# Performance work log

Measured on AMD Instinct MI355X. Metric: run time of the kernel, lower is better.

The kernel has to match this reference:

```python
import jax, jax.numpy as jnp
import numpy as np


def _gru(x, h, Wih, Whh, bih, bhh):
    # torch.nn.GRUCell math. x:(1,in), h:(1,H), Wih:(3H,in), Whh:(3H,H)
    gi = x @ Wih.T + bih
    gh = h @ Whh.T + bhh
    i_r, i_z, i_n = jnp.split(gi, 3, axis=-1)
    h_r, h_z, h_n = jnp.split(gh, 3, axis=-1)
    r = jax.nn.sigmoid(i_r + h_r)
    z = jax.nn.sigmoid(i_z + h_z)
    n = jnp.tanh(i_n + r * h_n)
    return (1.0 - z) * n + z * h


def _combine(S, Wa, ba, va):
    # SelfAttention.combine: additive attention over the stack axis.
    # S:(k,1,H), Wa:(H,A), ba:(A,), va:(A,)
    e = jnp.tanh(S @ Wa + ba) @ va          # (k,1) energies
    w = jax.nn.softmax(e, axis=0)            # softmax over stacked hidden states
    return jnp.sum(w[..., None] * S, axis=0)  # (1,H)


def setup_inputs() -> dict:
    key = jax.random.key(0)
    ks = jax.random.split(key, 20)
    T, F, H, A, L = 16384, 2048, 16, 64, 6
    G = 3 * H
    s = 0.1  # weight scale for numerical sanity
    return {
        "batch": jax.random.normal(ks[0], (T, 1, F), jnp.float32),
        "h0": jax.random.normal(ks[1], (L, 1, H), jnp.float32),
        "W_ih0": jax.random.normal(ks[2], (G, F), jnp.float32) * s,
        "W_hh0": jax.random.normal(ks[3], (G, H), jnp.float32) * s,
        "b_ih0": jax.random.normal(ks[4], (G,), jnp.float32) * s,
        "b_hh0": jax.random.normal(ks[5], (G,), jnp.float32) * s,
        "W_ih": jax.random.normal(ks[6], (L - 1, G, H), jnp.float32) * s,
        "W_hh": jax.random.normal(ks[7], (L - 1, G, H), jnp.float32) * s,
        "b_ih": jax.random.normal(ks[8], (L - 1, G), jnp.float32) * s,
        "b_hh": jax.random.normal(ks[9], (L - 1, G), jnp.float32) * s,
        "Wa": jax.random.normal(ks[10], (L, H, A), jnp.float32) * s,
        "ba": jax.random.normal(ks[11], (L, A), jnp.float32) * s,
        "va": jax.random.normal(ks[12], (L, A), jnp.float32) * s,
        "fc1_w": jax.random.normal(ks[13], (32, H), jnp.float32) * s,
        "fc1_b": jax.random.normal(ks[14], (32,), jnp.float32) * s,
        "fc2_w": jax.random.normal(ks[15], (1, 32), jnp.float32) * s,
        "fc2_b": jax.random.normal(ks[16], (1,), jnp.float32) * s,
    }


def reference(batch, h0, W_ih0, W_hh0, b_ih0, b_hh0, W_ih, W_hh, b_ih, b_hh,
              Wa, ba, va, fc1_w, fc1_b, fc2_w, fc2_b):
    L = Wa.shape[0]

    def step(h_s, x):
        # h_s: (L,1,H) carried hidden states, x: (1,F) current token
        inp = x.reshape(1, -1)
        new = []
        for l in range(L):
            if l == 0:
                inp = _gru(inp, h_s[0], W_ih0, W_hh0, b_ih0, b_hh0)
            else:
                inp = _gru(inp, h_s[l], W_ih[l - 1], W_hh[l - 1], b_ih[l - 1], b_hh[l - 1])
            new.append(inp)
        newS = jnp.stack(new)  # (L,1,H)
        # layer i attends over hidden states of layers i..L-1 (feedback combine)
        h_next = jnp.stack([_combine(newS[i:], Wa[i], ba[i], va[i]) for i in range(L)])
        top = h_next[-1].reshape(-1)  # (H,); dropout is identity in eval mode
        out = (top @ fc1_w.T + fc1_b) @ fc2_w.T + fc2_b  # (1,)
        return h_next, out

    _, outs = jax.lax.scan(step, h0, batch)
    return outs  # (T,1)
```

## Files before the change

kernel.cpp:

```cpp
#include <hip/hip_runtime.h>
#include <cstdint>
#include <cstddef>


#define TT 16384
#define FF 2048
#define HH 16
#define LL 6
#define GG 48
#define CHUNK 64
#define LOG2E 1.44269504088896340736f

__device__ float g_gi0p[(TT + CHUNK) * 64];

__device__ __forceinline__ float exp2_(float x) { return __builtin_amdgcn_exp2f(x); }
__device__ __forceinline__ float rcp_(float x) { return __builtin_amdgcn_rcpf(x); }
__device__ __forceinline__ float sig_n(float s) { return rcp_(1.f + exp2_(s)); }
__device__ __forceinline__ float tanh_p(float s) { return fmaf(-2.f, rcp_(exp2_(s) + 1.f), 1.f); }

#define MEMBAR() __asm__ __volatile__("" ::: "memory")

__device__ __forceinline__ float rdlane(float v, int l) {
  union { float f; int i; } a, b;
  a.f = v; b.i = __builtin_amdgcn_readlane(a.i, l); return b.f;
}
template <int CTRL>
__device__ __forceinline__ float dppf(float v) {
  union { float f; int i; } a, b;
  a.f = v; b.i = __builtin_amdgcn_mov_dpp(a.i, CTRL, 0xF, 0xF, true); return b.f;
}
template <int Q>
__device__ __forceinline__ float qbcast(float v) { return dppf<Q | (Q << 2) | (Q << 4) | (Q << 6)>(v); }

__device__ __forceinline__ float rowsum16(float v) {
  v += dppf<0xB1>(v);
  v += dppf<0x4E>(v);
  v += dppf<0x141>(v);
  v += dppf<0x140>(v);
  return v;
}
__device__ __forceinline__ float dot16r(const float (&w)[16], const float (&h)[16]) {
  float s0 = w[0] * h[0], s1 = w[1] * h[1], s2 = w[2] * h[2], s3 = w[3] * h[3];
#pragma unroll
  for (int k = 4; k < 16; k += 4) {
    s0 = fmaf(w[k], h[k], s0);       s1 = fmaf(w[k + 1], h[k + 1], s1);
    s2 = fmaf(w[k + 2], h[k + 2], s2); s3 = fmaf(w[k + 3], h[k + 3], s3);
  }
  return (s0 + s1) + (s2 + s3);
}
__device__ __forceinline__ float dot16i(const float (&w)[16], const float (&h)[16], float init) {
  float s0 = fmaf(w[0], h[0], init), s1 = w[1] * h[1], s2 = w[2] * h[2], s3 = w[3] * h[3];
#pragma unroll
  for (int k = 4; k < 16; k += 4) {
    s0 = fmaf(w[k], h[k], s0);       s1 = fmaf(w[k + 1], h[k + 1], s1);
    s2 = fmaf(w[k + 2], h[k + 2], s2); s3 = fmaf(w[k + 3], h[k + 3], s3);
  }
  return (s0 + s1) + (s2 + s3);
}

__device__ __forceinline__ int ldAcq(int* f) {
  return __hip_atomic_load(f, __ATOMIC_ACQUIRE, __HIP_MEMORY_SCOPE_WORKGROUP);
}
__device__ __forceinline__ void pollGE(int* f, int target) {
  while (ldAcq(f) < target) {}
}
__device__ __forceinline__ void waitFlag(int* f, int& cache, int need) {
  if (cache < need) { do { cache = ldAcq(f); } while (cache < need); }
}
__device__ __forceinline__ void sigRel(int* f, int v) {
  __hip_atomic_store(f, v, __ATOMIC_RELAXED, __HIP_MEMORY_SCOPE_WORKGROUP);
}

__device__ __forceinline__ void combBlock(const float4 A0, const float4 A1, const float4 A2,
                                          const float4 A3, float nsv,
                                          const float (&Wa)[16], float ba, float va,
                                          const float (&Wh)[16],
                                          float& S, float& ha, float& Pa) {
  float nr[16] = {A0.x, A0.y, A0.z, A0.w, A1.x, A1.y, A1.z, A1.w,
                  A2.x, A2.y, A2.z, A2.w, A3.x, A3.y, A3.z, A3.w};
  float u = dot16i(Wa, nr, ba);
  float P = dot16r(Wh, nr);
  float pe = va * tanh_p(u);
  float r = rowsum16(pe);
  float e = (rdlane(r, 0) + rdlane(r, 16)) + (rdlane(r, 32) + rdlane(r, 48));
  float w = exp2_(e);
  S += w; ha = fmaf(w, nsv, ha); Pa = fmaf(w, P, Pa);
}

__global__ __launch_bounds__(256) void gi0_gemm(const float* __restrict__ X,
                                                const float* __restrict__ W,
                                                const float* __restrict__ bias) {
  __shared__ float xs[64][132];
  __shared__ float ws[48][132];
  const int tid = threadIdx.x;
  const int t0 = blockIdx.x * 64;
  const int tg = tid & 15;
  const int tt = tid >> 4;
  float acc[4][3];
#pragma unroll
  for (int u = 0; u < 4; ++u)
#pragma unroll
    for (int v = 0; v < 3; ++v) acc[u][v] = 0.f;

  for (int k0 = 0; k0 < FF; k0 += 128) {
#pragma unroll
    for (int i = 0; i < 32; ++i) {
      int e = tid + 256 * i; int r = e >> 7, c = e & 127;
      xs[r][c] = X[(size_t)(t0 + r) * FF + k0 + c];
    }
#pragma unroll
    for (int i = 0; i < 24; ++i) {
      int e = tid + 256 * i; int r = e >> 7, c = e & 127;
      ws[r][c] = W[(size_t)r * FF + k0 + c];
    }
    __syncthreads();
#pragma unroll 8
    for (int c = 0; c < 128; ++c) {
      float x0 = xs[tt][c], x1 = xs[tt + 16][c], x2 = xs[tt + 32][c], x3 = xs[tt + 48][c];
      float w0 = ws[tg][c], w1 = ws[tg + 16][c], w2 = ws[tg + 32][c];
      acc[0][0] += x0 * w0; acc[0][1] += x0 * w1; acc[0][2] += x0 * w2;
      acc[1][0] += x1 * w0; acc[1][1] += x1 * w1; acc[1][2] += x1 * w2;
      acc[2][0] += x2 * w0; acc[2][1] += x2 * w1; acc[2][2] += x2 * w2;
      acc[3][0] += x3 * w0; acc[3][1] += x3 * w1; acc[3][2] += x3 * w2;
    }
    __syncthreads();
  }
  const float gsc3[3] = {-LOG2E, -LOG2E, 2.f * LOG2E};
#pragma unroll
  for (int u = 0; u < 4; ++u)
#pragma unroll
    for (int v = 0; v < 3; ++v)
      g_gi0p[(size_t)(t0 + tt + 16 * u) * 64 + tg * 4 + v] =
          (acc[u][v] + bias[tg + 16 * v]) * gsc3[v];
}

__global__ __launch_bounds__(512, 1) void fbrnn_scan(
    const float* __restrict__ h0,
    const float* __restrict__ Whh0, const float* __restrict__ bhh0,
    const float* __restrict__ Wih, const float* __restrict__ Whh,
    const float* __restrict__ bih, const float* __restrict__ bhh,
    const float* __restrict__ Wa, const float* __restrict__ ba,
    const float* __restrict__ va,
    const float* __restrict__ fc1w, const float* __restrict__ fc1b,
    const float* __restrict__ fc2w, const float* __restrict__ fc2b,
    float* __restrict__ out) {
  __shared__ __align__(16) float nsS[2][LL * HH];
  __shared__ __align__(16) float4 recS[5 * 64];
  __shared__ __align__(16) float4 partS[3 * 64];
  __shared__ __align__(16) float nsOut[256 * HH];
  __shared__ __align__(16) float chunkS[2][CHUNK * 64];
  __shared__ int flagNs;
  __shared__ int flagChunk;
  __shared__ int flagOut;
  __shared__ int gen5[2];

  const int tid = threadIdx.x;
  const int wv = tid >> 6;
  const int lane = tid & 63;
  const int qg = lane & 3;
  const int kk = lane >> 2;
  const int gate = (qg < 3 ? qg : 2);
  const int G = gate * 16 + kk;
  const float gsc = (gate == 2) ? 2.f * LOG2E : -LOG2E;

  const bool isChain = (wv == 0);
  const bool isStream = (wv == 4);
  const bool isFc = (wv == 6);
  const bool isComb = !isChain && !isStream && !isFc;
  const int pRow = (wv == 1) ? 0 : (wv == 2) ? 1 : (wv == 3) ? 2 : (wv == 7) ? 3 : 4;
  const int hRow = (wv == 5) ? 1 : (wv == 7) ? 2 : (wv == 6) ? 0 : -1;

  float WBih[5][16], bihR[5];
  float WB5[16];  float bhh5R = 0.f;
  float WaP[16], WhP[16];
  float baP = 0.f, vaP = 0.f, bhhP = 0.f;
  float WaH[16], WhH[16];
  float baH = 0.f, vaH = 0.f;
  float fc1R[16];
  float fb1 = 0.f, fw2 = 0.f, fb2 = 0.f;

  if (isChain) {
#pragma unroll
    for (int l = 0; l < 5; ++l) {
#pragma unroll
      for (int k = 0; k < 16; ++k) WBih[l][k] = Wih[((l * GG) + G) * 16 + k] * gsc;
      bihR[l] = bih[l * GG + G] * gsc;
    }
#pragma unroll
    for (int k = 0; k < 16; ++k) WB5[k] = Whh[(4 * GG + G) * 16 + k] * gsc;
    bhh5R = bhh[4 * GG + G] * gsc;
  }
  if (isComb) {
#pragma unroll
    for (int k = 0; k < 16; ++k) WaP[k] = Wa[(pRow * 16 + k) * 64 + lane] * (2.f * LOG2E);
    baP = ba[pRow * 64 + lane] * (2.f * LOG2E);
    vaP = va[pRow * 64 + lane] * LOG2E;
    const float* ws = (pRow == 0) ? (Whh0 + G * 16) : (Whh + ((pRow - 1) * GG + G) * 16);
#pragma unroll
    for (int k = 0; k < 16; ++k) WhP[k] = ws[k] * gsc;
    bhhP = ((pRow == 0) ? bhh0[G] : bhh[(pRow - 1) * GG + G]) * gsc;
  }
  if (hRow >= 0) {
#pragma unroll
    for (int k = 0; k < 16; ++k) WaH[k] = Wa[(hRow * 16 + k) * 64 + lane] * (2.f * LOG2E);
    baH = ba[hRow * 64 + lane] * (2.f * LOG2E);
    vaH = va[hRow * 64 + lane] * LOG2E;
    const float* ws = (hRow == 0) ? (Whh0 + G * 16) : (Whh + ((hRow - 1) * GG + G) * 16);
#pragma unroll
    for (int k = 0; k < 16; ++k) WhH[k] = ws[k] * gsc;
  }
  if (isFc) {
    const int m = lane & 31;
#pragma unroll
    for (int k = 0; k < 16; ++k) fc1R[k] = fc1w[m * 16 + k];
    fb1 = fc1b[m]; fw2 = fc2w[m]; fb2 = fc2b[0];
  }

  if (tid == 0) { flagNs = 0; flagChunk = 1; flagOut = 0; gen5[0] = 0; gen5[1] = 0; }

  float hv5 = 0.f, gh5reg = 0.f;
  if (isChain) {
    hv5 = h0[5 * 16 + kk];
    float hr[16];
#pragma unroll
    for (int k = 0; k < 16; ++k) hr[k] = h0[5 * 16 + k];
    gh5reg = dot16i(WB5, hr, bhh5R);
  } else if (isComb) {
    float hr[16];
#pragma unroll
    for (int k = 0; k < 16; ++k) hr[k] = h0[pRow * 16 + k];
    float4 rr;
    rr.x = dot16i(WhP, hr, bhhP);
    rr.y = h0[pRow * 16 + kk];
    rr.z = __int_as_float(0);
    rr.w = 0.f;
    recS[pRow * 64 + lane] = rr;
  } else if (isStream) {
    const float4* src = (const float4*)g_gi0p;
    float4* dst = (float4*)(&chunkS[0][0]);
#pragma unroll
    for (int q = 0; q < 16; ++q) dst[q * 64 + lane] = src[q * 64 + lane];
  }
  if (wv == 6) partS[0 * 64 + lane] = make_float4(0.f, 0.f, 0.f, __int_as_float(0));
  if (wv == 5) partS[1 * 64 + lane] = make_float4(0.f, 0.f, 0.f, __int_as_float(0));
  if (wv == 7) partS[2 * 64 + lane] = make_float4(0.f, 0.f, 0.f, __int_as_float(0));
  __syncthreads();

#define EBLOCK(J, WaX, baX, vaX, WhX, Sx, hax, Pax) do {                          \
    waitFlag(&flagNs, fcache, t * 8 + (J) + 1);                                   \
    const float4* np_ = (const float4*)&nsS[nb][(J) * 16];                        \
    float4 A0_ = np_[0], A1_ = np_[1], A2_ = np_[2], A3_ = np_[3];                \
    float nsv_ = nsS[nb][(J) * 16 + kk];                                          \
    combBlock(A0_, A1_, A2_, A3_, nsv_, WaX, baX, vaX, WhX, Sx, hax, Pax);        \
  } while (0)

  if (isStream) {
#pragma unroll 1
    for (int c = 1; c < 256; ++c) {
      if (c >= 2) pollGE(&flagNs, ((c - 1) * 64 - 1) * 8 + 1);
      const float4* src = (const float4*)(g_gi0p + ((size_t)c << 12));
      float4* dst = (float4*)(&chunkS[c & 1][0]);
#pragma unroll
      for (int q = 0; q < 16; ++q) dst[q * 64 + lane] = src[q * 64 + lane];
      MEMBAR();
      sigRel(&flagChunk, c + 1);
    }
    return;
  }

  if (isFc) {
    int fcache = 0;
#pragma unroll 1
    for (int t = 0; t < TT; ++t) {
      const int nb = t & 1;
      float Sh = 0.f, hah = 0.f, Pah = 0.f;
      EBLOCK(0, WaH, baH, vaH, WhH, Sh, hah, Pah);
      EBLOCK(1, WaH, baH, vaH, WhH, Sh, hah, Pah);
      EBLOCK(2, WaH, baH, vaH, WhH, Sh, hah, Pah);
      partS[0 * 64 + lane] = make_float4(Sh, hah, Pah, __int_as_float(t + 1));
      waitFlag(&flagNs, fcache, t * 8 + 6);
      const float4* np = (const float4*)(nsOut + (t & 255) * 16);
      float4 a0 = np[0], a1 = np[1], a2 = np[2], a3 = np[3];
      float nr[16] = {a0.x, a0.y, a0.z, a0.w, a1.x, a1.y, a1.z, a1.w,
                      a2.x, a2.y, a2.z, a2.w, a3.x, a3.y, a3.z, a3.w};
      float y = dot16i(fc1R, nr, fb1);
      float p = rowsum16(y * fw2);
      float o = rdlane(p, 0) + rdlane(p, 16) + fb2;
      if (lane == 0) out[t] = o;
      MEMBAR();
      sigRel(&flagOut, t + 1);
    }
    return;
  }

  if (isComb) {
    int fcache = 0;
    if (wv == 5) {
#pragma unroll 1
      for (int t = 0; t < TT; ++t) {
        const int nb = t & 1;
        const int tgt = t + 1;
        float Sh = 0.f, hah = 0.f, Pah = 0.f;
        EBLOCK(1, WaH, baH, vaH, WhH, Sh, hah, Pah);
        EBLOCK(2, WaH, baH, vaH, WhH, Sh, hah, Pah);
        partS[1 * 64 + lane] = make_float4(Sh, hah, Pah, __int_as_float(tgt));
        float S = 0.f, ha = 0.f, Pa = 0.f;
        EBLOCK(4, WaP, baP, vaP, WhP, S, ha, Pa);
        float4 A0, A1, A2, A3; float nsv5;
        for (;;) {
          int g5 = ldAcq(&gen5[nb]);
          MEMBAR();
          const float4* np = (const float4*)&nsS[nb][5 * 16];
          A0 = np[0]; A1 = np[1]; A2 = np[2]; A3 = np[3];
          nsv5 = nsS[nb][5 * 16 + kk];
          MEMBAR();
          if (g5 >= tgt) break;
        }
        combBlock(A0, A1, A2, A3, nsv5, WaP, baP, vaP, WhP, S, ha, Pa);
        const float inv = rcp_(S);
        float4 rr; rr.x = fmaf(Pa, inv, bhhP); rr.y = ha * inv;
        rr.z = __int_as_float(tgt); rr.w = 0.f;
        recS[4 * 64 + lane] = rr;
      }
    } else if (wv == 7) {
#pragma unroll 1
      for (int t = 0; t < TT; ++t) {
        const int nb = t & 1;
        const int tgt = t + 1;
        float Sh = 0.f, hah = 0.f, Pah = 0.f;
        EBLOCK(2, WaH, baH, vaH, WhH, Sh, hah, Pah);
        partS[2 * 64 + lane] = make_float4(Sh, hah, Pah, __int_as_float(tgt));
        float S = 0.f, ha = 0.f, Pa = 0.f;
        EBLOCK(3, WaP, baP, vaP, WhP, S, ha, Pa);
        EBLOCK(4, WaP, baP, vaP, WhP, S, ha, Pa);
        float4 A0, A1, A2, A3; float nsv5;
        for (;;) {
          int g5 = ldAcq(&gen5[nb]);
          MEMBAR();
          const float4* np = (const float4*)&nsS[nb][5 * 16];
          A0 = np[0]; A1 = np[1]; A2 = np[2]; A3 = np[3];
          nsv5 = nsS[nb][5 * 16 + kk];
          MEMBAR();
          if (g5 >= tgt) break;
        }
        combBlock(A0, A1, A2, A3, nsv5, WaP, baP, vaP, WhP, S, ha, Pa);
        const float inv = rcp_(S);
        float4 rr; rr.x = fmaf(Pa, inv, bhhP); rr.y = ha * inv;
        rr.z = __int_as_float(tgt); rr.w = 0.f;
        recS[3 * 64 + lane] = rr;
      }
    } else {
#pragma unroll 1
      for (int t = 0; t < TT; ++t) {
        const int nb = t & 1;
        const int tgt = t + 1;
        float S = 0.f, ha = 0.f, Pa = 0.f;
        EBLOCK(3, WaP, baP, vaP, WhP, S, ha, Pa);
        EBLOCK(4, WaP, baP, vaP, WhP, S, ha, Pa);
        float4 A0, A1, A2, A3, pp; float nsv5;
        for (;;) {
          int g5 = ldAcq(&gen5[nb]);
          MEMBAR();
          const float4* np = (const float4*)&nsS[nb][5 * 16];
          A0 = np[0]; A1 = np[1]; A2 = np[2]; A3 = np[3];
          nsv5 = nsS[nb][5 * 16 + kk];
          pp = partS[pRow * 64 + lane];
          MEMBAR();
          int pok = __all(__float_as_int(pp.w) >= tgt);
          if ((g5 >= tgt) & pok) break;
        }
        combBlock(A0, A1, A2, A3, nsv5, WaP, baP, vaP, WhP, S, ha, Pa);
        S += pp.x; ha += pp.y; Pa += pp.z;
        const float inv = rcp_(S);
        float4 rr; rr.x = fmaf(Pa, inv, bhhP); rr.y = ha * inv;
        rr.z = __int_as_float(tgt); rr.w = 0.f;
        recS[pRow * 64 + lane] = rr;
      }
    }
    return;
  }

  float gnext = chunkS[0][lane];
  float ns_sg[16];
#pragma unroll 1
  for (int t = 0; t < TT; ++t) {
    const int wb = t & 1;

    float4 r0, r1, r2, r3, r4;
    for (;;) {
      MEMBAR();
      r0 = recS[0 * 64 + lane]; r1 = recS[1 * 64 + lane]; r2 = recS[2 * 64 + lane];
      r3 = recS[3 * 64 + lane]; r4 = recS[4 * 64 + lane];
      MEMBAR();
      int c = (__float_as_int(r0.z) >= t) & (__float_as_int(r1.z) >= t) &
              (__float_as_int(r2.z) >= t) & (__float_as_int(r3.z) >= t) &
              (__float_as_int(r4.z) >= t);
      if (__all(c)) break;
    }
    float ghv[6], hv[6];
    ghv[0] = r0.x; hv[0] = r0.y; ghv[1] = r1.x; hv[1] = r1.y;
    ghv[2] = r2.x; hv[2] = r2.y; ghv[3] = r3.x; hv[3] = r3.y;
    ghv[4] = r4.x; hv[4] = r4.y;
    ghv[5] = gh5reg; hv[5] = hv5;

    if ((t & 63) == 63) {
      const int cn = (t + 1) >> 6;
      if (cn < 256) pollGE(&flagChunk, cn + 1);
    }
    if ((t & 63) == 32) pollGE(&flagOut, t - 64);
    const float gpre = chunkS[((t + 1) >> 6) & 1][((t + 1) & 63) * 64 + lane];

    float ghb[6];
#pragma unroll
    for (int l = 1; l < 6; ++l) ghb[l] = ghv[l] + bihR[l - 1];

    float gi0v = gnext;
    float ns = 0.f;
#pragma unroll
    for (int l = 0; l < 6; ++l) {
      const float gh_g = ghv[l];
      const float s = (l == 0) ? (gi0v + gh_g) : dot16i(WBih[l - 1], ns_sg, ghb[l]);
      const float sg = sig_n(s);
      const float smg = s - gh_g;
      const float sr = qbcast<0>(sg);
      const float sz = qbcast<1>(sg);
      const float a = sz * hv[l];
      const float b = 1.f - sz;
      const float tq = tanh_p(fmaf(sr, gh_g, smg));
      ns = fmaf(tq, b, a);
      if (qg == 2) {
        nsS[wb][l * 16 + kk] = ns;
        if (l == 5) nsOut[(t & 255) * 16 + kk] = ns;
      }
      MEMBAR();
      if (l == 5 && lane == 0) { sigRel(&gen5[wb], t + 1); sigRel(&flagNs, t * 8 + 6); }
#pragma unroll
      for (int k = 0; k < 16; ++k) ns_sg[k] = rdlane(ns, 4 * k + 2);
      if (l < 5 && lane == 0) sigRel(&flagNs, t * 8 + l + 1);
    }
    hv5 = qbcast<2>(ns);
    gh5reg = dot16i(WB5, ns_sg, bhh5R);
    gnext = gpre;
  }
}

extern "C" void kernel_launch(void* const* d_in, const int* in_sizes, int n_in,
                              void* d_out, int out_size, void* d_ws, size_t ws_size,
                              hipStream_t stream) {
  const float* batch = (const float*)d_in[0];
  const float* h0    = (const float*)d_in[1];
  const float* Wih0  = (const float*)d_in[2];
  const float* Whh0  = (const float*)d_in[3];
  const float* bih0  = (const float*)d_in[4];
  const float* bhh0  = (const float*)d_in[5];
  const float* Wih   = (const float*)d_in[6];
  const float* Whh   = (const float*)d_in[7];
  const float* bih   = (const float*)d_in[8];
  const float* bhh   = (const float*)d_in[9];
  const float* Wa    = (const float*)d_in[10];
  const float* ba    = (const float*)d_in[11];
  const float* va    = (const float*)d_in[12];
  const float* fc1w  = (const float*)d_in[13];
  const float* fc1b  = (const float*)d_in[14];
  const float* fc2w  = (const float*)d_in[15];
  const float* fc2b  = (const float*)d_in[16];
  float* out = (float*)d_out;
  (void)in_sizes; (void)n_in; (void)out_size; (void)d_ws; (void)ws_size;

  gi0_gemm<<<TT / 64, 256, 0, stream>>>(batch, Wih0, bih0);
  fbrnn_scan<<<1, 512, 0, stream>>>(h0, Whh0, bhh0, Wih, Whh, bih, bhh,
                                    Wa, ba, va, fc1w, fc1b, fc2w, fc2b, out);
}
```

Baseline: 24.99 ms.

## Finalize combine rows 0-1 in chain wave and rebalance partial-sum waves

Moves the final attention-combine step for rows 0 and 1 into the chain wave itself, using the layer-5 state it just computed plus partial sums posted by helper waves. This removes the handoff through shared memory for the rows needed first in the next timestep. The remaining row readiness checks are deferred until layer 2, and the chunk and output polls are moved after layer 0, so waiting overlaps with compute. The bih biases are also folded into the recurrent biases ahead of time. In exchange the chain wave does more per-step work and holds more registers, and the wave-to-row assignments are reshuffled.

```diff
diff --git a/kernel.cpp b/kernel.cpp
--- a/kernel.cpp
+++ b/kernel.cpp
@@ -146,7 +146,7 @@
     float* __restrict__ out) {
   __shared__ __align__(16) float nsS[2][LL * HH];
   __shared__ __align__(16) float4 recS[5 * 64];
-  __shared__ __align__(16) float4 partS[3 * 64];
+  __shared__ __align__(16) float4 partS[4 * 64];
   __shared__ __align__(16) float nsOut[256 * HH];
   __shared__ __align__(16) float chunkS[2][CHUNK * 64];
   __shared__ int flagNs;
@@ -166,12 +166,15 @@
   const bool isChain = (wv == 0);
   const bool isStream = (wv == 4);
   const bool isFc = (wv == 6);
-  const bool isComb = !isChain && !isStream && !isFc;
-  const int pRow = (wv == 1) ? 0 : (wv == 2) ? 1 : (wv == 3) ? 2 : (wv == 7) ? 3 : 4;
-  const int hRow = (wv == 5) ? 1 : (wv == 7) ? 2 : (wv == 6) ? 0 : -1;
-
-  float WBih[5][16], bihR[5];
+  const int hRow = (wv == 6 || wv == 1) ? 0 : (wv == 2 || wv == 5) ? 1 : -1;
+  const int pRow = (wv == 3) ? 2 : (wv == 7) ? 3 : (wv == 5) ? 4 : -1;
+  const int pSlot = (wv == 6) ? 0 : (wv == 1) ? 1 : (wv == 2) ? 2 : (wv == 5) ? 3 : -1;
+
+  float WBih[5][16];
   float WB5[16];  float bhh5R = 0.f;
+  float Wa0R[16], Wh0R[16], Wa1R[16], Wh1R[16];
+  float ba0R = 0.f, va0R = 0.f, bb0 = 0.f;
+  float ba1R = 0.f, va1R = 0.f, bb1 = 0.f;
   float WaP[16], WhP[16];
   float baP = 0.f, vaP = 0.f, bhhP = 0.f;
   float WaH[16], WhH[16];
@@ -181,24 +184,33 @@
 
   if (isChain) {
 #pragma unroll
-    for (int l = 0; l < 5; ++l) {
+    for (int l = 0; l < 5; ++l)
 #pragma unroll
       for (int k = 0; k < 16; ++k) WBih[l][k] = Wih[((l * GG) + G) * 16 + k] * gsc;
-      bihR[l] = bih[l * GG + G] * gsc;
-    }
 #pragma unroll
     for (int k = 0; k < 16; ++k) WB5[k] = Whh[(4 * GG + G) * 16 + k] * gsc;
-    bhh5R = bhh[4 * GG + G] * gsc;
-  }
-  if (isComb) {
+    bhh5R = (bhh[4 * GG + G] + bih[4 * GG + G]) * gsc;
+#pragma unroll
+    for (int k = 0; k < 16; ++k) {
+      Wa0R[k] = Wa[(0 * 16 + k) * 64 + lane] * (2.f * LOG2E);
+      Wa1R[k] = Wa[(1 * 16 + k) * 64 + lane] * (2.f * LOG2E);
+      Wh0R[k] = Whh0[G * 16 + k] * gsc;
+      Wh1R[k] = Whh[(0 * GG + G) * 16 + k] * gsc;
+    }
+    ba0R = ba[0 * 64 + lane] * (2.f * LOG2E); va0R = va[0 * 64 + lane] * LOG2E;
+    ba1R = ba[1 * 64 + lane] * (2.f * LOG2E); va1R = va[1 * 64 + lane] * LOG2E;
+    bb0 = bhh0[G] * gsc;
+    bb1 = (bhh[0 * GG + G] + bih[0 * GG + G]) * gsc;
+  }
+  if (pRow >= 0) {
 #pragma unroll
     for (int k = 0; k < 16; ++k) WaP[k] = Wa[(pRow * 16 + k) * 64 + lane] * (2.f * LOG2E);
     baP = ba[pRow * 64 + lane] * (2.f * LOG2E);
     vaP = va[pRow * 64 + lane] * LOG2E;
-    const float* ws = (pRow == 0) ? (Whh0 + G * 16) : (Whh + ((pRow - 1) * GG + G) * 16);
+    const float* ws = Whh + ((pRow - 1) * GG + G) * 16;
 #pragma unroll
     for (int k = 0; k < 16; ++k) WhP[k] = ws[k] * gsc;
-    bhhP = ((pRow == 0) ? bhh0[G] : bhh[(pRow - 1) * GG + G]) * gsc;
+    bhhP = (bhh[(pRow - 1) * GG + G] + bih[(pRow - 1) * GG + G]) * gsc;
   }
   if (hRow >= 0) {
 #pragma unroll
@@ -219,13 +231,22 @@
   if (tid == 0) { flagNs = 0; flagChunk = 1; flagOut = 0; gen5[0] = 0; gen5[1] = 0; }
 
   float hv5 = 0.f, gh5reg = 0.f;
+  float gh0n = 0.f, hv0n = 0.f, gh1n = 0.f, hv1n = 0.f;
   if (isChain) {
+    float hr[16];
+#pragma unroll
+    for (int k = 0; k < 16; ++k) hr[k] = h0[5 * 16 + k];
     hv5 = h0[5 * 16 + kk];
-    float hr[16];
-#pragma unroll
-    for (int k = 0; k < 16; ++k) hr[k] = h0[5 * 16 + k];
     gh5reg = dot16i(WB5, hr, bhh5R);
-  } else if (isComb) {
+#pragma unroll
+    for (int k = 0; k < 16; ++k) hr[k] = h0[0 * 16 + k];
+    hv0n = h0[0 * 16 + kk];
+    gh0n = dot16i(Wh0R, hr, bb0);
+#pragma unroll
+    for (int k = 0; k < 16; ++k) hr[k] = h0[1 * 16 + k];
+    hv1n = h0[1 * 16 + kk];
+    gh1n = dot16i(Wh1R, hr, bb1);
+  } else if (pRow >= 0) {
     float hr[16];
 #pragma unroll
     for (int k = 0; k < 16; ++k) hr[k] = h0[pRow * 16 + k];
@@ -235,15 +256,14 @@
     rr.z = __int_as_float(0);
     rr.w = 0.f;
     recS[pRow * 64 + lane] = rr;
-  } else if (isStream) {
+  }
+  if (isStream) {
     const float4* src = (const float4*)g_gi0p;
     float4* dst = (float4*)(&chunkS[0][0]);
 #pragma unroll
     for (int q = 0; q < 16; ++q) dst[q * 64 + lane] = src[q * 64 + lane];
   }
-  if (wv == 6) partS[0 * 64 + lane] = make_float4(0.f, 0.f, 0.f, __int_as_float(0));
-  if (wv == 5) partS[1 * 64 + lane] = make_float4(0.f, 0.f, 0.f, __int_as_float(0));
-  if (wv == 7) partS[2 * 64 + lane] = make_float4(0.f, 0.f, 0.f, __int_as_float(0));
+  if (pSlot >= 0) partS[pSlot * 64 + lane] = make_float4(0.f, 0.f, 0.f, __int_as_float(0));
   __syncthreads();
 
 #define EBLOCK(J, WaX, baX, vaX, WhX, Sx, hax, Pax) do {                          \
@@ -252,6 +272,24 @@
     float4 A0_ = np_[0], A1_ = np_[1], A2_ = np_[2], A3_ = np_[3];                \
     float nsv_ = nsS[nb][(J) * 16 + kk];                                          \
     combBlock(A0_, A1_, A2_, A3_, nsv_, WaX, baX, vaX, WhX, Sx, hax, Pax);        \
+  } while (0)
+
+#define TAILFIN(ROW, Sv, hav, Pav) do {                                           \
+    float4 A0, A1, A2, A3; float nsv5;                                            \
+    for (;;) {                                                                    \
+      int g5 = ldAcq(&gen5[nb]);                                                  \
+      MEMBAR();                                                                   \
+      const float4* np = (const float4*)&nsS[nb][5 * 16];                         \
+      A0 = np[0]; A1 = np[1]; A2 = np[2]; A3 = np[3];                             \
+      nsv5 = nsS[nb][5 * 16 + kk];                                                \
+      MEMBAR();                                                                   \
+      if (g5 >= tgt) break;                                                       \
+    }                                                                             \
+    combBlock(A0, A1, A2, A3, nsv5, WaP, baP, vaP, WhP, Sv, hav, Pav);            \
+    const float inv_ = rcp_(Sv);                                                  \
+    float4 rr_; rr_.x = fmaf(Pav, inv_, bhhP); rr_.y = hav * inv_;                \
+    rr_.z = __int_as_float(tgt); rr_.w = 0.f;                                     \
+    recS[(ROW) * 64 + lane] = rr_;                                                \
   } while (0)
 
   if (isStream) {
@@ -293,61 +331,49 @@
     return;
   }
 
-  if (isComb) {
+  if (!isChain) {
     int fcache = 0;
-    if (wv == 5) {
+    if (wv == 1) {
+#pragma unroll 1
+      for (int t = 0; t < TT; ++t) {
+        const int nb = t & 1;
+        float Sh = 0.f, hah = 0.f, Pah = 0.f;
+        EBLOCK(3, WaH, baH, vaH, WhH, Sh, hah, Pah);
+        EBLOCK(4, WaH, baH, vaH, WhH, Sh, hah, Pah);
+        partS[1 * 64 + lane] = make_float4(Sh, hah, Pah, __int_as_float(t + 1));
+      }
+    } else if (wv == 2) {
+#pragma unroll 1
+      for (int t = 0; t < TT; ++t) {
+        const int nb = t & 1;
+        float Sh = 0.f, hah = 0.f, Pah = 0.f;
+        EBLOCK(1, WaH, baH, vaH, WhH, Sh, hah, Pah);
+        EBLOCK(2, WaH, baH, vaH, WhH, Sh, hah, Pah);
+        EBLOCK(3, WaH, baH, vaH, WhH, Sh, hah, Pah);
+        partS[2 * 64 + lane] = make_float4(Sh, hah, Pah, __int_as_float(t + 1));
+      }
+    } else if (wv == 5) {
 #pragma unroll 1
       for (int t = 0; t < TT; ++t) {
         const int nb = t & 1;
         const int tgt = t + 1;
         float Sh = 0.f, hah = 0.f, Pah = 0.f;
-        EBLOCK(1, WaH, baH, vaH, WhH, Sh, hah, Pah);
-        EBLOCK(2, WaH, baH, vaH, WhH, Sh, hah, Pah);
-        partS[1 * 64 + lane] = make_float4(Sh, hah, Pah, __int_as_float(tgt));
+        EBLOCK(4, WaH, baH, vaH, WhH, Sh, hah, Pah);
+        partS[3 * 64 + lane] = make_float4(Sh, hah, Pah, __int_as_float(tgt));
         float S = 0.f, ha = 0.f, Pa = 0.f;
         EBLOCK(4, WaP, baP, vaP, WhP, S, ha, Pa);
-        float4 A0, A1, A2, A3; float nsv5;
-        for (;;) {
-          int g5 = ldAcq(&gen5[nb]);
-          MEMBAR();
-          const float4* np = (const float4*)&nsS[nb][5 * 16];
-          A0 = np[0]; A1 = np[1]; A2 = np[2]; A3 = np[3];
-          nsv5 = nsS[nb][5 * 16 + kk];
-          MEMBAR();
-          if (g5 >= tgt) break;
-        }
-        combBlock(A0, A1, A2, A3, nsv5, WaP, baP, vaP, WhP, S, ha, Pa);
-        const float inv = rcp_(S);
-        float4 rr; rr.x = fmaf(Pa, inv, bhhP); rr.y = ha * inv;
-        rr.z = __int_as_float(tgt); rr.w = 0.f;
-        recS[4 * 64 + lane] = rr;
-      }
-    } else if (wv == 7) {
+        TAILFIN(4, S, ha, Pa);
+      }
+    } else if (wv == 3) {
 #pragma unroll 1
       for (int t = 0; t < TT; ++t) {
         const int nb = t & 1;
         const int tgt = t + 1;
-        float Sh = 0.f, hah = 0.f, Pah = 0.f;
-        EBLOCK(2, WaH, baH, vaH, WhH, Sh, hah, Pah);
-        partS[2 * 64 + lane] = make_float4(Sh, hah, Pah, __int_as_float(tgt));
         float S = 0.f, ha = 0.f, Pa = 0.f;
+        EBLOCK(2, WaP, baP, vaP, WhP, S, ha, Pa);
         EBLOCK(3, WaP, baP, vaP, WhP, S, ha, Pa);
         EBLOCK(4, WaP, baP, vaP, WhP, S, ha, Pa);
-        float4 A0, A1, A2, A3; float nsv5;
-        for (;;) {
-          int g5 = ldAcq(&gen5[nb]);
-          MEMBAR();
-          const float4* np = (const float4*)&nsS[nb][5 * 16];
-          A0 = np[0]; A1 = np[1]; A2 = np[2]; A3 = np[3];
-          nsv5 = nsS[nb][5 * 16 + kk];
-          MEMBAR();
-          if (g5 >= tgt) break;
-        }
-        combBlock(A0, A1, A2, A3, nsv5, WaP, baP, vaP, WhP, S, ha, Pa);
-        const float inv = rcp_(S);
-        float4 rr; rr.x = fmaf(Pa, inv, bhhP); rr.y = ha * inv;
-        rr.z = __int_as_float(tgt); rr.w = 0.f;
-        recS[3 * 64 + lane] = rr;
+        TAILFIN(2, S, ha, Pa);
       }
     } else {
 #pragma unroll 1
@@ -357,24 +383,7 @@
         float S = 0.f, ha = 0.f, Pa = 0.f;
         EBLOCK(3, WaP, baP, vaP, WhP, S, ha, Pa);
         EBLOCK(4, WaP, baP, vaP, WhP, S, ha, Pa);
-        float4 A0, A1, A2, A3, pp; float nsv5;
-        for (;;) {
-          int g5 = ldAcq(&gen5[nb]);
-          MEMBAR();
-          const float4* np = (const float4*)&nsS[nb][5 * 16];
-          A0 = np[0]; A1 = np[1]; A2 = np[2]; A3 = np[3];
-          nsv5 = nsS[nb][5 * 16 + kk];
-          pp = partS[pRow * 64 + lane];
-          MEMBAR();
-          int pok = __all(__float_as_int(pp.w) >= tgt);
-          if ((g5 >= tgt) & pok) break;
-        }
-        combBlock(A0, A1, A2, A3, nsv5, WaP, baP, vaP, WhP, S, ha, Pa);
-        S += pp.x; ha += pp.y; Pa += pp.z;
-        const float inv = rcp_(S);
-        float4 rr; rr.x = fmaf(Pa, inv, bhhP); rr.y = ha * inv;
-        rr.z = __int_as_float(tgt); rr.w = 0.f;
-        recS[pRow * 64 + lane] = rr;
+        TAILFIN(3, S, ha, Pa);
       }
     }
     return;
@@ -386,40 +395,32 @@
   for (int t = 0; t < TT; ++t) {
     const int wb = t & 1;
 
-    float4 r0, r1, r2, r3, r4;
-    for (;;) {
-      MEMBAR();
-      r0 = recS[0 * 64 + lane]; r1 = recS[1 * 64 + lane]; r2 = recS[2 * 64 + lane];
-      r3 = recS[3 * 64 + lane]; r4 = recS[4 * 64 + lane];
-      MEMBAR();
-      int c = (__float_as_int(r0.z) >= t) & (__float_as_int(r1.z) >= t) &
-              (__float_as_int(r2.z) >= t) & (__float_as_int(r3.z) >= t) &
-              (__float_as_int(r4.z) >= t);
-      if (__all(c)) break;
-    }
     float ghv[6], hv[6];
-    ghv[0] = r0.x; hv[0] = r0.y; ghv[1] = r1.x; hv[1] = r1.y;
-    ghv[2] = r2.x; hv[2] = r2.y; ghv[3] = r3.x; hv[3] = r3.y;
-    ghv[4] = r4.x; hv[4] = r4.y;
+    ghv[0] = gh0n; hv[0] = hv0n;
+    ghv[1] = gh1n; hv[1] = hv1n;
     ghv[5] = gh5reg; hv[5] = hv5;
-
-    if ((t & 63) == 63) {
-      const int cn = (t + 1) >> 6;
-      if (cn < 256) pollGE(&flagChunk, cn + 1);
-    }
-    if ((t & 63) == 32) pollGE(&flagOut, t - 64);
-    const float gpre = chunkS[((t + 1) >> 6) & 1][((t + 1) & 63) * 64 + lane];
-
-    float ghb[6];
-#pragma unroll
-    for (int l = 1; l < 6; ++l) ghb[l] = ghv[l] + bihR[l - 1];
-
+    float4 r2, r3, r4;
+    float gpre = 0.f;
     float gi0v = gnext;
     float ns = 0.f;
 #pragma unroll
     for (int l = 0; l < 6; ++l) {
+      if (l == 2) {
+        if (!((__float_as_int(r2.z) >= t) & (__float_as_int(r3.z) >= t) &
+              (__float_as_int(r4.z) >= t))) {
+          do {
+            MEMBAR();
+            r2 = recS[2 * 64 + lane]; r3 = recS[3 * 64 + lane]; r4 = recS[4 * 64 + lane];
+            MEMBAR();
+          } while (!((__float_as_int(r2.z) >= t) & (__float_as_int(r3.z) >= t) &
+                     (__float_as_int(r4.z) >= t)));
+        }
+        ghv[2] = r2.x; hv[2] = r2.y;
+        ghv[3] = r3.x; hv[3] = r3.y;
+        ghv[4] = r4.x; hv[4] = r4.y;
+      }
       const float gh_g = ghv[l];
-      const float s = (l == 0) ? (gi0v + gh_g) : dot16i(WBih[l - 1], ns_sg, ghb[l]);
+      const float s = (l == 0) ? (gi0v + gh_g) : dot16i(WBih[l - 1], ns_sg, gh_g);
       const float sg = sig_n(s);
       const float smg = s - gh_g;
       const float sr = qbcast<0>(sg);
@@ -437,9 +438,57 @@
 #pragma unroll
       for (int k = 0; k < 16; ++k) ns_sg[k] = rdlane(ns, 4 * k + 2);
       if (l < 5 && lane == 0) sigRel(&flagNs, t * 8 + l + 1);
-    }
-    hv5 = qbcast<2>(ns);
+      if (l == 0) {
+        if ((t & 63) == 63) {
+          const int cn = (t + 1) >> 6;
+          if (cn < 256) pollGE(&flagChunk, cn + 1);
+        }
+        if ((t & 63) == 32) pollGE(&flagOut, t - 64);
+        gpre = chunkS[((t + 1) >> 6) & 1][((t + 1) & 63) * 64 + lane];
+        MEMBAR();
+        r2 = recS[2 * 64 + lane]; r3 = recS[3 * 64 + lane]; r4 = recS[4 * 64 + lane];
+        MEMBAR();
+      }
+    }
+    const float hv5n = qbcast<2>(ns);
     gh5reg = dot16i(WB5, ns_sg, bhh5R);
+    float u0 = dot16i(Wa0R, ns_sg, ba0R);
+    float u1 = dot16i(Wa1R, ns_sg, ba1R);
+    float P0 = dot16r(Wh0R, ns_sg);
+    float P1 = dot16r(Wh1R, ns_sg);
+    MEMBAR();
+    float4 p0a = partS[0 * 64 + lane], p0b = partS[1 * 64 + lane];
+    float4 p1a = partS[2 * 64 + lane], p1b = partS[3 * 64 + lane];
+    MEMBAR();
+    float pe0 = va0R * tanh_p(u0);
+    float pe1 = va1R * tanh_p(u1);
+    float rs0 = rowsum16(pe0);
+    float rs1 = rowsum16(pe1);
+    float e0 = (rdlane(rs0, 0) + rdlane(rs0, 16)) + (rdlane(rs0, 32) + rdlane(rs0, 48));
+    float e1 = (rdlane(rs1, 0) + rdlane(rs1, 16)) + (rdlane(rs1, 32) + rdlane(rs1, 48));
+    float wj0 = exp2_(e0), wj1 = exp2_(e1);
+    const int tp = t + 1;
+    if (!((__float_as_int(p0a.w) >= tp) & (__float_as_int(p0b.w) >= tp) &
+          (__float_as_int(p1a.w) >= tp) & (__float_as_int(p1b.w) >= tp))) {
+      do {
+        MEMBAR();
+        p0a = partS[0 * 64 + lane]; p0b = partS[1 * 64 + lane];
+        p1a = partS[2 * 64 + lane]; p1b = partS[3 * 64 + lane];
+        MEMBAR();
+      } while (!((__float_as_int(p0a.w) >= tp) & (__float_as_int(p0b.w) >= tp) &
+                 (__float_as_int(p1a.w) >= tp) & (__float_as_int(p1b.w) >= tp)));
+    }
+    float S0 = p0a.x + p0b.x + wj0;
+    float hT0 = p0a.y + p0b.y + wj0 * hv5n;
+    float PT0 = p0a.z + p0b.z + wj0 * P0;
+    float S1 = p1a.x + p1b.x + wj1;
+    float hT1 = p1a.y + p1b.y + wj1 * hv5n;
+    float PT1 = p1a.z + p1b.z + wj1 * P1;
+    const float inv0 = rcp_(S0);
+    const float inv1 = rcp_(S1);
+    gh0n = fmaf(PT0, inv0, bb0); hv0n = hT0 * inv0;
+    gh1n = fmaf(PT1, inv1, bb1); hv1n = hT1 * inv1;
+    hv5 = hv5n;
     gnext = gpre;
   }
 }
```

New measurement: 22.11 ms. -11.5%, faster.
